# Performance work log

Hardware: AMD Instinct MI355X
Metric: run time of the kernel (lower is better)

The kernel has to match this reference:

```python
import jax, jax.numpy as jnp
import numpy as np

N_POOL = 500_000   # number of source neurons (value store size)
N_W = 1024         # number of unique (deduplicated) weight matrices
E = 1_000_000      # number of connections (neuron-input pairs)
D_IN = 16
D_OUT = 16


def setup_inputs() -> dict:
    key = jax.random.key(0)
    k1, k2, k3, k4 = jax.random.split(key, 4)
    values = jax.random.normal(k1, (N_POOL, D_IN), dtype=jnp.float32)
    weight = jax.random.normal(k2, (N_W, D_OUT, D_IN), dtype=jnp.float32)
    input_idx = jax.random.randint(k3, (E,), 0, N_POOL, dtype=jnp.int64) if jax.config.jax_enable_x64 else jax.random.randint(k3, (E,), 0, N_POOL).astype(jnp.int32)
    weight_idx = jax.random.randint(k4, (E,), 0, N_W).astype(jnp.int32)
    return {"values": values, "weight": weight, "input_idx": input_idx, "weight_idx": weight_idx}


def reference(values, weight, input_idx, weight_idx):
    # LINEAR_GATHER: gather input value vectors per connection  -> [E, D_IN]
    x = values[input_idx]
    # LINEAR_WEIGHTS_GATHER: gather weight matrices per connection -> [E, D_OUT, D_IN]
    w = weight[weight_idx]
    # LINEAR_LINEAR: per-connection matmul (w @ input_values) -> [E, D_OUT]
    y = jnp.einsum('eoi,ei->eo', w, x)
    return y
```

## Files before the change

### kernel.cpp

```cpp
#include <hip/hip_runtime.h>


#define D 16
#define NWMAX 1024
#define NB 256
#define BTS 1024
#define SEGB 4

__global__ __launch_bounds__(256) void linear_gather_mv(
    const float* __restrict__ values, const float* __restrict__ weight,
    const int* __restrict__ input_idx, const int* __restrict__ weight_idx,
    float* __restrict__ out, int E)
{
    int tid = blockIdx.x * blockDim.x + threadIdx.x;
    int e = tid >> 2;
    int j = tid & 3;
    if (e >= E) return;
    int ii = input_idx[e];
    int wi = weight_idx[e];
    const float4* xp = (const float4*)(values + (long long)ii * D);
    float4 x0 = xp[0], x1 = xp[1], x2 = xp[2], x3 = xp[3];
    const float4* wp = (const float4*)(weight + (long long)wi * (D * D) + j * (4 * D));
    float4 acc;
    float* accp = (float*)&acc;
    #pragma unroll
    for (int r = 0; r < 4; ++r) {
        float4 w0 = wp[r * 4 + 0], w1 = wp[r * 4 + 1], w2 = wp[r * 4 + 2], w3 = wp[r * 4 + 3];
        accp[r] = w0.x * x0.x + w0.y * x0.y + w0.z * x0.z + w0.w * x0.w
                + w1.x * x1.x + w1.y * x1.y + w1.z * x1.z + w1.w * x1.w
                + w2.x * x2.x + w2.y * x2.y + w2.z * x2.z + w2.w * x2.w
                + w3.x * x3.x + w3.y * x3.y + w3.z * x3.z + w3.w * x3.w;
    }
    ((float4*)out)[(long long)e * 4 + j] = acc;
}

__global__ __launch_bounds__(BTS) void hist_blocks(
    const int* __restrict__ widx, int E, int chunk,
    int* __restrict__ hist2d, int NW)
{
    __shared__ int lh[NWMAX];
    for (int i = threadIdx.x; i < NW; i += BTS) lh[i] = 0;
    __syncthreads();
    int s0 = blockIdx.x * chunk;
    int s1 = min(E, s0 + chunk);
    for (int e = s0 + threadIdx.x; e < s1; e += BTS)
        atomicAdd(&lh[widx[e]], 1);
    __syncthreads();
    int* row = hist2d + (long long)blockIdx.x * NW;
    for (int i = threadIdx.x; i < NW; i += BTS) row[i] = lh[i];
}

__global__ __launch_bounds__(NB) void scan_per_bin(
    int* __restrict__ hist2d, int* __restrict__ total, int NW)
{
    __shared__ int buf[2 * NB];
    int b = blockIdx.x;
    int t = threadIdx.x;
    int v = hist2d[(long long)t * NW + b];
    buf[t] = v;
    __syncthreads();
    int pin = 0;
    for (int off = 1; off < NB; off <<= 1) {
        int x = buf[pin * NB + t];
        if (t >= off) x += buf[pin * NB + t - off];
        buf[(1 - pin) * NB + t] = x;
        pin = 1 - pin;
        __syncthreads();
    }
    int incl = buf[pin * NB + t];
    hist2d[(long long)t * NW + b] = incl - v;
    if (t == NB - 1) total[b] = incl;
}

__global__ __launch_bounds__(1024) void scan_bins(
    const int* __restrict__ total, int* __restrict__ offsets, int NW)
{
    __shared__ int buf[2 * NWMAX];
    int t = threadIdx.x;
    int v = (t < NW) ? total[t] : 0;
    buf[t] = v;
    __syncthreads();
    int pin = 0;
    for (int off = 1; off < NWMAX; off <<= 1) {
        int x = buf[pin * NWMAX + t];
        if (t >= off) x += buf[pin * NWMAX + t - off];
        buf[(1 - pin) * NWMAX + t] = x;
        pin = 1 - pin;
        __syncthreads();
    }
    int incl = buf[pin * NWMAX + t];
    if (t < NW) {
        offsets[t + 1] = incl;
        if (t == 0) offsets[0] = 0;
    }
}

__global__ __launch_bounds__(BTS) void scatter_det(
    const int* __restrict__ widx, const int* __restrict__ iidx, int E, int chunk,
    const int* __restrict__ hist2d, const int* __restrict__ offsets,
    int2* __restrict__ perm, int NW)
{
    __shared__ int cur[NWMAX];
    int p = blockIdx.x;
    const int* row = hist2d + (long long)p * NW;
    for (int i = threadIdx.x; i < NW; i += BTS)
        cur[i] = offsets[i] + row[i];
    __syncthreads();
    int s0 = p * chunk;
    int s1 = min(E, s0 + chunk);
    for (int e = s0 + threadIdx.x; e < s1; e += BTS) {
        int wi = widx[e];
        int pos = atomicAdd(&cur[wi], 1);
        perm[pos] = make_int2(e, iidx[e]);
    }
}

#define ROWDOT(X0, X1, X2, X3)                                   \
    (w0.x*X0.x + w0.y*X0.y + w0.z*X0.z + w0.w*X0.w               \
   + w1.x*X1.x + w1.y*X1.y + w1.z*X1.z + w1.w*X1.w               \
   + w2.x*X2.x + w2.y*X2.y + w2.z*X2.z + w2.w*X2.w               \
   + w3.x*X3.x + w3.y*X3.y + w3.z*X3.z + w3.w*X3.w)

__global__ __launch_bounds__(64) void bucket_mv(
    const float* __restrict__ values, const float* __restrict__ weight,
    const int* __restrict__ offsets, const int2* __restrict__ perm,
    float* __restrict__ out)
{
    __shared__ float xbuf[64 * D];
    int b = blockIdx.x;
    int lo = offsets[b], hi = offsets[b + 1];
    int cnt = hi - lo;
    if (cnt == 0) return;
    int per = (cnt + SEGB - 1) / SEGB;
    int s0 = lo + blockIdx.y * per;
    int s1 = min(hi, s0 + per);
    if (s0 >= s1) return;

    int lane = threadIdx.x;
    int sg   = lane >> 4;
    int i    = lane & 15;
    int g4   = lane >> 2;
    int q    = lane & 3;

    const float4* wr = (const float4*)(weight + (long long)b * (D * D) + i * D);
    float4 w0 = wr[0], w1 = wr[1], w2 = wr[2], w3 = wr[3];
    asm volatile("" : "+v"(w0.x), "+v"(w0.y), "+v"(w0.z), "+v"(w0.w),
                      "+v"(w1.x), "+v"(w1.y), "+v"(w1.z), "+v"(w1.w),
                      "+v"(w2.x), "+v"(w2.y), "+v"(w2.z), "+v"(w2.w),
                      "+v"(w3.x), "+v"(w3.y), "+v"(w3.z), "+v"(w3.w));

    int2 pe;
    float4 xq0, xq1, xq2, xq3;
    {
        int kl = s0 + lane; if (kl >= s1) kl = s1 - 1;
        pe = perm[kl];
        int iiu;
        iiu = __shfl(pe.y,       g4); xq0 = ((const float4*)(values + (long long)iiu * D))[q];
        iiu = __shfl(pe.y, 16 +  g4); xq1 = ((const float4*)(values + (long long)iiu * D))[q];
        iiu = __shfl(pe.y, 32 +  g4); xq2 = ((const float4*)(values + (long long)iiu * D))[q];
        iiu = __shfl(pe.y, 48 +  g4); xq3 = ((const float4*)(values + (long long)iiu * D))[q];
    }

    for (int k0 = s0; k0 < s1; k0 += 64) {
        ((float4*)&xbuf[( 0 + g4) * D])[q ^ 0] = xq0;
        ((float4*)&xbuf[(16 + g4) * D])[q ^ 1] = xq1;
        ((float4*)&xbuf[(32 + g4) * D])[q ^ 2] = xq2;
        ((float4*)&xbuf[(48 + g4) * D])[q ^ 3] = xq3;
        int2 pe_cur = pe;
        int nb = s1 - k0; if (nb > 64) nb = 64;

        int kn = k0 + 64;
        if (kn < s1) {
            int kl = kn + lane; if (kl >= s1) kl = s1 - 1;
            pe = perm[kl];
            int iiu;
            iiu = __shfl(pe.y,       g4); xq0 = ((const float4*)(values + (long long)iiu * D))[q];
            iiu = __shfl(pe.y, 16 +  g4); xq1 = ((const float4*)(values + (long long)iiu * D))[q];
            iiu = __shfl(pe.y, 32 +  g4); xq2 = ((const float4*)(values + (long long)iiu * D))[q];
            iiu = __shfl(pe.y, 48 +  g4); xq3 = ((const float4*)(values + (long long)iiu * D))[q];
        }

        #pragma unroll 4
        for (int t = 0; t < 16; ++t) {
            int iw2 = sg * 16 + t;
            const float4* xr = (const float4*)&xbuf[iw2 * D];
            float4 x0 = xr[sg ^ 0];
            float4 x1 = xr[sg ^ 1];
            float4 x2 = xr[sg ^ 2];
            float4 x3 = xr[sg ^ 3];
            float y = ROWDOT(x0, x1, x2, x3);
            int e_t = __shfl(pe_cur.x, iw2);
            if (iw2 < nb)
                out[(long long)e_t * D + i] = y;
        }
    }
}

extern "C" void kernel_launch(void* const* d_in, const int* in_sizes, int n_in,
                              void* d_out, int out_size, void* d_ws, size_t ws_size,
                              hipStream_t stream) {
    const float* values     = (const float*)d_in[0];
    const float* weight     = (const float*)d_in[1];
    const int*   input_idx  = (const int*)d_in[2];
    const int*   weight_idx = (const int*)d_in[3];
    float*       out        = (float*)d_out;

    int E  = in_sizes[2];
    int NW = in_sizes[1] / (D * D);
    int chunk = (E + NB - 1) / NB;

    size_t n_hist = (size_t)NB * NW;
    size_t n_head = n_hist + NW + NW + 1;
    n_head = (n_head + 1) & ~(size_t)1;
    size_t need = (n_head + 2 * (size_t)E) * sizeof(int);

    if (NW > NWMAX || ws_size < need) {
        int total_thr = E * 4;
        int grid = (total_thr + 255) / 256;
        hipLaunchKernelGGL(linear_gather_mv, dim3(grid), dim3(256), 0, stream,
                           values, weight, input_idx, weight_idx, out, E);
        return;
    }

    int* hist2d  = (int*)d_ws;
    int* total   = hist2d + n_hist;
    int* offsets = total + NW;
    int2* perm   = (int2*)((int*)d_ws + n_head);

    hipLaunchKernelGGL(hist_blocks, dim3(NB), dim3(BTS), 0, stream,
                       weight_idx, E, chunk, hist2d, NW);
    hipLaunchKernelGGL(scan_per_bin, dim3(NW), dim3(NB), 0, stream,
                       hist2d, total, NW);
    hipLaunchKernelGGL(scan_bins, dim3(1), dim3(1024), 0, stream,
                       total, offsets, NW);
    hipLaunchKernelGGL(scatter_det, dim3(NB), dim3(BTS), 0, stream,
                       weight_idx, input_idx, E, chunk, hist2d, offsets, perm, NW);
    hipLaunchKernelGGL(bucket_mv, dim3(NW, SEGB), dim3(64), 0, stream,
                       values, weight, offsets, perm, out);
}
```

Baseline: 146.5 us.

## Replace sort-by-weight pipeline with single direct gather kernel using cached weight loads

Drops the five-kernel pipeline that bucketed connections by weight index (histogram, two scans, scatter, bucketed matvec) and runs one kernel over connections in their original order. Each wave stages 64 input vectors in shared memory, then for every connection loads one float4 of that connection's 1KB weight matrix per lane, relying on L2 to hold the 1MB weight table. Row dot products are reduced with xor shuffles, and weight loads are double-buffered in groups of eight. This removes the sort's extra passes and its workspace traffic, at the cost of reading a full weight matrix per connection from cache and writing output with scalar stores from a quarter of the lanes.

```diff
diff --git a/kernel.cpp b/kernel.cpp
--- a/kernel.cpp
+++ b/kernel.cpp
@@ -2,163 +2,63 @@
 
 
 #define D 16
-#define NWMAX 1024
-#define NB 256
-#define BTS 1024
-#define SEGB 4
+#define BPB 4
 
-__global__ __launch_bounds__(256) void linear_gather_mv(
+__device__ __forceinline__ float4 wload(const float* __restrict__ weight,
+                                        int wi, int lane) {
+    return ((const float4*)(weight + (long long)wi * (D * D)))[lane];
+}
+
+#define WLOAD8(C0, W0,W1,W2,W3,W4,W5,W6,W7) do {                               \
+    W0 = wload(weight, __builtin_amdgcn_readlane(wcur, (C0)+0), lane);         \
+    W1 = wload(weight, __builtin_amdgcn_readlane(wcur, (C0)+1), lane);         \
+    W2 = wload(weight, __builtin_amdgcn_readlane(wcur, (C0)+2), lane);         \
+    W3 = wload(weight, __builtin_amdgcn_readlane(wcur, (C0)+3), lane);         \
+    W4 = wload(weight, __builtin_amdgcn_readlane(wcur, (C0)+4), lane);         \
+    W5 = wload(weight, __builtin_amdgcn_readlane(wcur, (C0)+5), lane);         \
+    W6 = wload(weight, __builtin_amdgcn_readlane(wcur, (C0)+6), lane);         \
+    W7 = wload(weight, __builtin_amdgcn_readlane(wcur, (C0)+7), lane);         \
+} while (0)
+
+#define CONN1(C, WV) do {                                                      \
+    const float4 xv = *(const float4*)(&xbuf[(C) * D + ((q ^ ((C) >> 4)) << 2)]); \
+    float p = WV.x*xv.x + WV.y*xv.y + WV.z*xv.z + WV.w*xv.w;                   \
+    p += __shfl_xor(p, 1);                                                     \
+    p += __shfl_xor(p, 2);                                                     \
+    if (q == 0 && (C) < nb) out[(long long)(k0 + (C)) * D + r] = p;            \
+} while (0)
+
+#define CONN8(C0, W0,W1,W2,W3,W4,W5,W6,W7) do {                                \
+    CONN1((C0)+0, W0); CONN1((C0)+1, W1); CONN1((C0)+2, W2); CONN1((C0)+3, W3);\
+    CONN1((C0)+4, W4); CONN1((C0)+5, W5); CONN1((C0)+6, W6); CONN1((C0)+7, W7);\
+} while (0)
+
+__global__ __launch_bounds__(64, 4) void direct_mv(
     const float* __restrict__ values, const float* __restrict__ weight,
-    const int* __restrict__ input_idx, const int* __restrict__ weight_idx,
+    const int* __restrict__ iidx, const int* __restrict__ widx,
     float* __restrict__ out, int E)
 {
-    int tid = blockIdx.x * blockDim.x + threadIdx.x;
-    int e = tid >> 2;
-    int j = tid & 3;
-    if (e >= E) return;
-    int ii = input_idx[e];
-    int wi = weight_idx[e];
-    const float4* xp = (const float4*)(values + (long long)ii * D);
-    float4 x0 = xp[0], x1 = xp[1], x2 = xp[2], x3 = xp[3];
-    const float4* wp = (const float4*)(weight + (long long)wi * (D * D) + j * (4 * D));
-    float4 acc;
-    float* accp = (float*)&acc;
-    #pragma unroll
-    for (int r = 0; r < 4; ++r) {
-        float4 w0 = wp[r * 4 + 0], w1 = wp[r * 4 + 1], w2 = wp[r * 4 + 2], w3 = wp[r * 4 + 3];
-        accp[r] = w0.x * x0.x + w0.y * x0.y + w0.z * x0.z + w0.w * x0.w
-                + w1.x * x1.x + w1.y * x1.y + w1.z * x1.z + w1.w * x1.w
-                + w2.x * x2.x + w2.y * x2.y + w2.z * x2.z + w2.w * x2.w
-                + w3.x * x3.x + w3.y * x3.y + w3.z * x3.z + w3.w * x3.w;
-    }
-    ((float4*)out)[(long long)e * 4 + j] = acc;
-}
+    __shared__ float xbuf[64 * D];
+    const int lane = threadIdx.x;
+    const int g4 = lane >> 2;
+    const int q  = lane & 3;
+    const int r  = g4;
 
-__global__ __launch_bounds__(BTS) void hist_blocks(
-    const int* __restrict__ widx, int E, int chunk,
-    int* __restrict__ hist2d, int NW)
-{
-    __shared__ int lh[NWMAX];
-    for (int i = threadIdx.x; i < NW; i += BTS) lh[i] = 0;
-    __syncthreads();
-    int s0 = blockIdx.x * chunk;
-    int s1 = min(E, s0 + chunk);
-    for (int e = s0 + threadIdx.x; e < s1; e += BTS)
-        atomicAdd(&lh[widx[e]], 1);
-    __syncthreads();
-    int* row = hist2d + (long long)blockIdx.x * NW;
-    for (int i = threadIdx.x; i < NW; i += BTS) row[i] = lh[i];
-}
+    int s0 = blockIdx.x * (64 * BPB);
+    if (s0 >= E) return;
+    int s1 = min(E, s0 + 64 * BPB);
 
-__global__ __launch_bounds__(NB) void scan_per_bin(
-    int* __restrict__ hist2d, int* __restrict__ total, int NW)
-{
-    __shared__ int buf[2 * NB];
-    int b = blockIdx.x;
-    int t = threadIdx.x;
-    int v = hist2d[(long long)t * NW + b];
-    buf[t] = v;
-    __syncthreads();
-    int pin = 0;
-    for (int off = 1; off < NB; off <<= 1) {
-        int x = buf[pin * NB + t];
-        if (t >= off) x += buf[pin * NB + t - off];
-        buf[(1 - pin) * NB + t] = x;
-        pin = 1 - pin;
-        __syncthreads();
-    }
-    int incl = buf[pin * NB + t];
-    hist2d[(long long)t * NW + b] = incl - v;
-    if (t == NB - 1) total[b] = incl;
-}
-
-__global__ __launch_bounds__(1024) void scan_bins(
-    const int* __restrict__ total, int* __restrict__ offsets, int NW)
-{
-    __shared__ int buf[2 * NWMAX];
-    int t = threadIdx.x;
-    int v = (t < NW) ? total[t] : 0;
-    buf[t] = v;
-    __syncthreads();
-    int pin = 0;
-    for (int off = 1; off < NWMAX; off <<= 1) {
-        int x = buf[pin * NWMAX + t];
-        if (t >= off) x += buf[pin * NWMAX + t - off];
-        buf[(1 - pin) * NWMAX + t] = x;
-        pin = 1 - pin;
-        __syncthreads();
-    }
-    int incl = buf[pin * NWMAX + t];
-    if (t < NW) {
-        offsets[t + 1] = incl;
-        if (t == 0) offsets[0] = 0;
-    }
-}
-
-__global__ __launch_bounds__(BTS) void scatter_det(
-    const int* __restrict__ widx, const int* __restrict__ iidx, int E, int chunk,
-    const int* __restrict__ hist2d, const int* __restrict__ offsets,
-    int2* __restrict__ perm, int NW)
-{
-    __shared__ int cur[NWMAX];
-    int p = blockIdx.x;
-    const int* row = hist2d + (long long)p * NW;
-    for (int i = threadIdx.x; i < NW; i += BTS)
-        cur[i] = offsets[i] + row[i];
-    __syncthreads();
-    int s0 = p * chunk;
-    int s1 = min(E, s0 + chunk);
-    for (int e = s0 + threadIdx.x; e < s1; e += BTS) {
-        int wi = widx[e];
-        int pos = atomicAdd(&cur[wi], 1);
-        perm[pos] = make_int2(e, iidx[e]);
-    }
-}
-
-#define ROWDOT(X0, X1, X2, X3)                                   \
-    (w0.x*X0.x + w0.y*X0.y + w0.z*X0.z + w0.w*X0.w               \
-   + w1.x*X1.x + w1.y*X1.y + w1.z*X1.z + w1.w*X1.w               \
-   + w2.x*X2.x + w2.y*X2.y + w2.z*X2.z + w2.w*X2.w               \
-   + w3.x*X3.x + w3.y*X3.y + w3.z*X3.z + w3.w*X3.w)
-
-__global__ __launch_bounds__(64) void bucket_mv(
-    const float* __restrict__ values, const float* __restrict__ weight,
-    const int* __restrict__ offsets, const int2* __restrict__ perm,
-    float* __restrict__ out)
-{
-    __shared__ float xbuf[64 * D];
-    int b = blockIdx.x;
-    int lo = offsets[b], hi = offsets[b + 1];
-    int cnt = hi - lo;
-    if (cnt == 0) return;
-    int per = (cnt + SEGB - 1) / SEGB;
-    int s0 = lo + blockIdx.y * per;
-    int s1 = min(hi, s0 + per);
-    if (s0 >= s1) return;
-
-    int lane = threadIdx.x;
-    int sg   = lane >> 4;
-    int i    = lane & 15;
-    int g4   = lane >> 2;
-    int q    = lane & 3;
-
-    const float4* wr = (const float4*)(weight + (long long)b * (D * D) + i * D);
-    float4 w0 = wr[0], w1 = wr[1], w2 = wr[2], w3 = wr[3];
-    asm volatile("" : "+v"(w0.x), "+v"(w0.y), "+v"(w0.z), "+v"(w0.w),
-                      "+v"(w1.x), "+v"(w1.y), "+v"(w1.z), "+v"(w1.w),
-                      "+v"(w2.x), "+v"(w2.y), "+v"(w2.z), "+v"(w2.w),
-                      "+v"(w3.x), "+v"(w3.y), "+v"(w3.z), "+v"(w3.w));
-
-    int2 pe;
+    int iv, wnext;
     float4 xq0, xq1, xq2, xq3;
     {
         int kl = s0 + lane; if (kl >= s1) kl = s1 - 1;
-        pe = perm[kl];
+        iv    = iidx[kl];
+        wnext = widx[kl];
         int iiu;
-        iiu = __shfl(pe.y,       g4); xq0 = ((const float4*)(values + (long long)iiu * D))[q];
-        iiu = __shfl(pe.y, 16 +  g4); xq1 = ((const float4*)(values + (long long)iiu * D))[q];
-        iiu = __shfl(pe.y, 32 +  g4); xq2 = ((const float4*)(values + (long long)iiu * D))[q];
-        iiu = __shfl(pe.y, 48 +  g4); xq3 = ((const float4*)(values + (long long)iiu * D))[q];
+        iiu = __shfl(iv,      g4); xq0 = ((const float4*)(values + (long long)iiu * D))[q];
+        iiu = __shfl(iv, 16 + g4); xq1 = ((const float4*)(values + (long long)iiu * D))[q];
+        iiu = __shfl(iv, 32 + g4); xq2 = ((const float4*)(values + (long long)iiu * D))[q];
+        iiu = __shfl(iv, 48 + g4); xq3 = ((const float4*)(values + (long long)iiu * D))[q];
     }
 
     for (int k0 = s0; k0 < s1; k0 += 64) {
@@ -166,33 +66,39 @@
         ((float4*)&xbuf[(16 + g4) * D])[q ^ 1] = xq1;
         ((float4*)&xbuf[(32 + g4) * D])[q ^ 2] = xq2;
         ((float4*)&xbuf[(48 + g4) * D])[q ^ 3] = xq3;
-        int2 pe_cur = pe;
+        int wcur = wnext;
         int nb = s1 - k0; if (nb > 64) nb = 64;
 
         int kn = k0 + 64;
         if (kn < s1) {
             int kl = kn + lane; if (kl >= s1) kl = s1 - 1;
-            pe = perm[kl];
+            iv    = iidx[kl];
+            wnext = widx[kl];
             int iiu;
-            iiu = __shfl(pe.y,       g4); xq0 = ((const float4*)(values + (long long)iiu * D))[q];
-            iiu = __shfl(pe.y, 16 +  g4); xq1 = ((const float4*)(values + (long long)iiu * D))[q];
-            iiu = __shfl(pe.y, 32 +  g4); xq2 = ((const float4*)(values + (long long)iiu * D))[q];
-            iiu = __shfl(pe.y, 48 +  g4); xq3 = ((const float4*)(values + (long long)iiu * D))[q];
+            iiu = __shfl(iv,      g4); xq0 = ((const float4*)(values + (long long)iiu * D))[q];
+            iiu = __shfl(iv, 16 + g4); xq1 = ((const float4*)(values + (long long)iiu * D))[q];
+            iiu = __shfl(iv, 32 + g4); xq2 = ((const float4*)(values + (long long)iiu * D))[q];
+            iiu = __shfl(iv, 48 + g4); xq3 = ((const float4*)(values + (long long)iiu * D))[q];
         }
 
-        #pragma unroll 4
-        for (int t = 0; t < 16; ++t) {
-            int iw2 = sg * 16 + t;
-            const float4* xr = (const float4*)&xbuf[iw2 * D];
-            float4 x0 = xr[sg ^ 0];
-            float4 x1 = xr[sg ^ 1];
-            float4 x2 = xr[sg ^ 2];
-            float4 x3 = xr[sg ^ 3];
-            float y = ROWDOT(x0, x1, x2, x3);
-            int e_t = __shfl(pe_cur.x, iw2);
-            if (iw2 < nb)
-                out[(long long)e_t * D + i] = y;
-        }
+        float4 A0,A1,A2,A3,A4,A5,A6,A7;
+        float4 B0,B1,B2,B3,B4,B5,B6,B7;
+        WLOAD8( 0, A0,A1,A2,A3,A4,A5,A6,A7);
+        WLOAD8( 8, B0,B1,B2,B3,B4,B5,B6,B7);
+        CONN8 ( 0, A0,A1,A2,A3,A4,A5,A6,A7);
+        WLOAD8(16, A0,A1,A2,A3,A4,A5,A6,A7);
+        CONN8 ( 8, B0,B1,B2,B3,B4,B5,B6,B7);
+        WLOAD8(24, B0,B1,B2,B3,B4,B5,B6,B7);
+        CONN8 (16, A0,A1,A2,A3,A4,A5,A6,A7);
+        WLOAD8(32, A0,A1,A2,A3,A4,A5,A6,A7);
+        CONN8 (24, B0,B1,B2,B3,B4,B5,B6,B7);
+        WLOAD8(40, B0,B1,B2,B3,B4,B5,B6,B7);
+        CONN8 (32, A0,A1,A2,A3,A4,A5,A6,A7);
+        WLOAD8(48, A0,A1,A2,A3,A4,A5,A6,A7);
+        CONN8 (40, B0,B1,B2,B3,B4,B5,B6,B7);
+        WLOAD8(56, B0,B1,B2,B3,B4,B5,B6,B7);
+        CONN8 (48, A0,A1,A2,A3,A4,A5,A6,A7);
+        CONN8 (56, B0,B1,B2,B3,B4,B5,B6,B7);
     }
 }
 
@@ -205,36 +111,9 @@
     const int*   weight_idx = (const int*)d_in[3];
     float*       out        = (float*)d_out;
 
-    int E  = in_sizes[2];
-    int NW = in_sizes[1] / (D * D);
-    int chunk = (E + NB - 1) / NB;
-
-    size_t n_hist = (size_t)NB * NW;
-    size_t n_head = n_hist + NW + NW + 1;
-    n_head = (n_head + 1) & ~(size_t)1;
-    size_t need = (n_head + 2 * (size_t)E) * sizeof(int);
-
-    if (NW > NWMAX || ws_size < need) {
-        int total_thr = E * 4;
-        int grid = (total_thr + 255) / 256;
-        hipLaunchKernelGGL(linear_gather_mv, dim3(grid), dim3(256), 0, stream,
-                           values, weight, input_idx, weight_idx, out, E);
-        return;
-    }
-
-    int* hist2d  = (int*)d_ws;
-    int* total   = hist2d + n_hist;
-    int* offsets = total + NW;
-    int2* perm   = (int2*)((int*)d_ws + n_head);
-
-    hipLaunchKernelGGL(hist_blocks, dim3(NB), dim3(BTS), 0, stream,
-                       weight_idx, E, chunk, hist2d, NW);
-    hipLaunchKernelGGL(scan_per_bin, dim3(NW), dim3(NB), 0, stream,
-                       hist2d, total, NW);
-    hipLaunchKernelGGL(scan_bins, dim3(1), dim3(1024), 0, stream,
-                       total, offsets, NW);
-    hipLaunchKernelGGL(scatter_det, dim3(NB), dim3(BTS), 0, stream,
-                       weight_idx, input_idx, E, chunk, hist2d, offsets, perm, NW);
-    hipLaunchKernelGGL(bucket_mv, dim3(NW, SEGB), dim3(64), 0, stream,
-                       values, weight, offsets, perm, out);
+    int E = in_sizes[2];
+    if (E <= 0) return;
+    int nblk = (E + 64 * BPB - 1) / (64 * BPB);
+    hipLaunchKernelGGL(direct_mv, dim3(nblk), dim3(64), 0, stream,
+                       values, weight, input_idx, weight_idx, out, E);
 }
```

Result: slower. 150.7 us (+2.8%).
